# Optimization experiments

Hardware: AMD Instinct MI355X
Metric: run time of the kernel (lower is better)

## Reference

```python
import jax, jax.numpy as jnp
import numpy as np


def setup_inputs() -> dict:
    key = jax.random.key(0)
    k1, k2, k3, k4, k5 = jax.random.split(key, 5)
    B, n_vis, n_hid, n_target = 16384, 2048, 512, 2
    return {
        "input_data": jax.random.normal(k1, (B, n_vis), dtype=jnp.float32),
        "W": jax.random.normal(k2, (n_hid, n_vis), dtype=jnp.float32),
        "U": jax.random.normal(k3, (n_hid, n_target), dtype=jnp.float32),
        "h_bias": jax.random.normal(k4, (1, n_hid), dtype=jnp.float32),
        "y_bias": jax.random.normal(k5, (1, n_target), dtype=jnp.float32),
    }


def reference(input_data, W, U, h_bias, y_bias):
    # precomputed_factor: [B, n_hid]
    pf = input_data @ W.T + h_bias
    # logits[b, c] = y_bias[c] + sum_j softplus(pf[b, j] + U[j, c])
    # broadcast to [B, n_hid, n_target], reduce over hidden dim
    sp = jax.nn.softplus(pf[:, :, None] + U[None, :, :])  # [B, n_hid, n_target]
    logits = y_bias + sp.sum(axis=1)  # [B, n_target]
    # the double class loop computes 1 / sum_d exp(logits_d - logits_c) == softmax
    return jax.nn.softmax(logits, axis=1)
```

## Files before the change

kernel.cpp:

```cpp
#include <hip/hip_runtime.h>
#include <hip/hip_bf16.h>
#include <hip/hip_fp16.h>
#include <stdint.h>

typedef __attribute__((ext_vector_type(8))) _Float16 f16x8;
typedef __attribute__((ext_vector_type(4))) float f32x4;
typedef __attribute__((ext_vector_type(4))) int i32x4;

#define GLD_LDS16(g, l) __builtin_amdgcn_global_load_lds( \
    (const __attribute__((address_space(1))) uint32_t*)(g), \
    (__attribute__((address_space(3))) uint32_t*)(l), 16, 0, 0)

__global__ __launch_bounds__(256) void k_cvt_w(const float* __restrict__ W,
                                               _Float16* __restrict__ Wh) {
  int i = (blockIdx.x * 256 + threadIdx.x) * 8;
  float4 a = *(const float4*)(W + i);
  float4 b = *(const float4*)(W + i + 4);
  union { _Float16 h[8]; i32x4 v; } u;
  u.h[0] = (_Float16)a.x; u.h[1] = (_Float16)a.y;
  u.h[2] = (_Float16)a.z; u.h[3] = (_Float16)a.w;
  u.h[4] = (_Float16)b.x; u.h[5] = (_Float16)b.y;
  u.h[6] = (_Float16)b.z; u.h[7] = (_Float16)b.w;
  *(i32x4*)(Wh + i) = u.v;
}

__device__ inline float softplus_f(float x) {
  float e = __expf(-fabsf(x));
  return fmaxf(x, 0.f) + __logf(1.f + e);
}

__global__ __launch_bounds__(512, 2) void k_main(
    const float* __restrict__ X,
    const _Float16* __restrict__ Wh,
    const float* __restrict__ U,
    const float* __restrict__ hb,
    float* __restrict__ Dp) {
  __shared__ __align__(16) _Float16 As[2][128 * 64];
  __shared__ __align__(16) _Float16 Bs[3][256 * 64];
  __shared__ float sD[128];

  const int t = threadIdx.x;
  const int lane = t & 63;
  const int wid = t >> 6;
  const int wm = wid >> 2;
  const int wn = wid & 3;
  const int bx = blockIdx.x;
  const int rt = (bx >> 4) * 8 + (bx & 7);
  const int nhalf = (bx >> 3) & 1;
  const int bm0 = rt * 128;
  const int bn0 = nhalf * 256;
  const int lrow = lane & 15, lq = lane >> 4;

  if (t < 128) sD[t] = 0.f;
  __syncthreads();

  f32x4 acc[4][4];
#pragma unroll
  for (int m = 0; m < 4; ++m)
#pragma unroll
    for (int n = 0; n < 4; ++n) acc[m][n] = (f32x4){0.f, 0.f, 0.f, 0.f};

  const int arow = t >> 2, ach = t & 3;
  const float* xsrc = X + (size_t)(bm0 + arow) * 2048 + ach * 16;
  const int c0 = ach * 2;
  const int aw0 = arow * 128 + (((c0) ^ (arow & 7)) << 4);
  const int aw1 = arow * 128 + (((c0 + 1) ^ (arow & 7)) << 4);

  const int l8 = lane >> 3, s8 = lane & 7;
  const _Float16* bsrc =
      Wh + (size_t)(bn0 + wid * 32 + l8) * 2048 + (s8 ^ l8) * 8;
  char* const bd0 = (char*)&Bs[0][0] + wid * 4096;
  char* const bd1 = (char*)&Bs[1][0] + wid * 4096;
  char* const bd2 = (char*)&Bs[2][0] + wid * 4096;

  f32x4 arA[4], arB[4];

#define CVT_WRITE_A(ARC, Q) do {                                           \
    f16x8 hv0, hv1;                                                        \
    _Pragma("unroll") for (int j = 0; j < 4; ++j) {                        \
      hv0[j] = (_Float16)ARC[0][j]; hv0[j + 4] = (_Float16)ARC[1][j];      \
      hv1[j] = (_Float16)ARC[2][j]; hv1[j + 4] = (_Float16)ARC[3][j];      \
    }                                                                      \
    *(f16x8*)((char*)&As[Q][0] + aw0) = hv0;                               \
    *(f16x8*)((char*)&As[Q][0] + aw1) = hv1;                               \
  } while (0)

#define STEP(KT, P, Q, ARL, ARC, BR, BWD) do {                             \
    const int kb_ = ((KT) + 2 > 31) ? 31 : (KT) + 2;                       \
    _Pragma("unroll") for (int i = 0; i < 4; ++i)                          \
      GLD_LDS16(bsrc + (size_t)i * 16384 + (size_t)kb_ * 64,               \
                (BWD) + i * 1024);                                         \
    _Pragma("unroll") for (int c = 0; c < 4; ++c)                          \
      ARL[c] = *(const f32x4*)(xsrc + (size_t)kb_ * 64 + c * 4);           \
    CVT_WRITE_A(ARC, Q);                                                   \
    f16x8 fa[4][2], fb[4][2];                                              \
    _Pragma("unroll") for (int mf = 0; mf < 4; ++mf) {                     \
      int row = wm * 64 + mf * 16 + lrow;                                  \
      _Pragma("unroll") for (int ks = 0; ks < 2; ++ks) {                   \
        int off = row * 128 + (((ks * 4 + lq) ^ (row & 7)) << 4);          \
        fa[mf][ks] = *(const f16x8*)((const char*)&As[P][0] + off);        \
      }                                                                    \
    }                                                                      \
    _Pragma("unroll") for (int nf = 0; nf < 4; ++nf) {                     \
      int row = wn * 64 + nf * 16 + lrow;                                  \
      _Pragma("unroll") for (int ks = 0; ks < 2; ++ks) {                   \
        int off = row * 128 + (((ks * 4 + lq) ^ (row & 7)) << 4);          \
        fb[nf][ks] = *(const f16x8*)((const char*)&Bs[BR][0] + off);       \
      }                                                                    \
    }                                                                      \
    _Pragma("unroll") for (int ks = 0; ks < 2; ++ks)                       \
      _Pragma("unroll") for (int mf = 0; mf < 4; ++mf)                     \
        _Pragma("unroll") for (int nf = 0; nf < 4; ++nf)                   \
          acc[mf][nf] = __builtin_amdgcn_mfma_f32_16x16x32_f16(            \
              fa[mf][ks], fb[nf][ks], acc[mf][nf], 0, 0, 0);               \
    asm volatile("s_waitcnt vmcnt(8) lgkmcnt(0)" ::: "memory");            \
    __builtin_amdgcn_s_barrier();                                          \
  } while (0)

#pragma unroll
  for (int i = 0; i < 4; ++i)
    GLD_LDS16(bsrc + (size_t)i * 16384, bd0 + i * 1024);
#pragma unroll
  for (int i = 0; i < 4; ++i)
    GLD_LDS16(bsrc + (size_t)i * 16384 + 64, bd1 + i * 1024);
#pragma unroll
  for (int c = 0; c < 4; ++c) arA[c] = *(const f32x4*)(xsrc + c * 4);
#pragma unroll
  for (int c = 0; c < 4; ++c) arB[c] = *(const f32x4*)(xsrc + 64 + c * 4);
  CVT_WRITE_A(arA, 0);
  asm volatile("s_waitcnt vmcnt(4) lgkmcnt(0)" ::: "memory");
  __builtin_amdgcn_s_barrier();

  for (int kt = 0; kt < 30; kt += 6) {
    STEP(kt + 0, 0, 1, arA, arB, 0, bd2);
    STEP(kt + 1, 1, 0, arB, arA, 1, bd0);
    STEP(kt + 2, 0, 1, arA, arB, 2, bd1);
    STEP(kt + 3, 1, 0, arB, arA, 0, bd2);
    STEP(kt + 4, 0, 1, arA, arB, 1, bd0);
    STEP(kt + 5, 1, 0, arB, arA, 2, bd1);
  }
  STEP(30, 0, 1, arA, arB, 0, bd2);
  STEP(31, 1, 0, arB, arA, 1, bd0);
#undef STEP
#undef CVT_WRITE_A

  float dpart[16];
#pragma unroll
  for (int i = 0; i < 16; ++i) dpart[i] = 0.f;
#pragma unroll
  for (int nf = 0; nf < 4; ++nf) {
    int h = bn0 + wn * 64 + nf * 16 + lrow;
    float hbv = hb[h];
    float u0 = U[2 * h], u1 = U[2 * h + 1];
#pragma unroll
    for (int mf = 0; mf < 4; ++mf)
#pragma unroll
      for (int r = 0; r < 4; ++r) {
        float pf = acc[mf][nf][r] + hbv;
        dpart[mf * 4 + r] += softplus_f(pf + u0) - softplus_f(pf + u1);
      }
  }
#pragma unroll
  for (int i = 0; i < 16; ++i) {
    float v = dpart[i];
    v += __shfl_xor(v, 1);
    v += __shfl_xor(v, 2);
    v += __shfl_xor(v, 4);
    v += __shfl_xor(v, 8);
    dpart[i] = v;
  }
  if (lrow == 0) {
#pragma unroll
    for (int mf = 0; mf < 4; ++mf)
#pragma unroll
      for (int r = 0; r < 4; ++r)
        atomicAdd(&sD[wm * 64 + mf * 16 + lq * 4 + r], dpart[mf * 4 + r]);
  }
  __syncthreads();
  if (t < 128) Dp[nhalf * 16384 + bm0 + t] = sD[t];
}

__global__ __launch_bounds__(256) void k_final(const float* __restrict__ Dp,
                                               const float* __restrict__ yb,
                                               float* __restrict__ out) {
  int i = blockIdx.x * 256 + threadIdx.x;
  float D = Dp[i] + Dp[16384 + i] + yb[0] - yb[1];
  float e = __expf(-D);
  float o0 = 1.f / (1.f + e);
  float o1 = e * o0;
  *(float2*)(out + (size_t)i * 2) = make_float2(o0, o1);
}

extern "C" void kernel_launch(void* const* d_in, const int* in_sizes, int n_in,
                              void* d_out, int out_size, void* d_ws,
                              size_t ws_size, hipStream_t stream) {
  const float* X = (const float*)d_in[0];
  const float* W = (const float*)d_in[1];
  const float* U = (const float*)d_in[2];
  const float* hb = (const float*)d_in[3];
  const float* yb = (const float*)d_in[4];
  float* out = (float*)d_out;
  _Float16* Wh = (_Float16*)d_ws;
  float* Dp = (float*)((char*)d_ws + 2 * 1024 * 1024);

  hipLaunchKernelGGL(k_cvt_w, dim3(512), dim3(256), 0, stream, W, Wh);
  hipLaunchKernelGGL(k_main, dim3(256), dim3(512), 0, stream, X, Wh, U, hb, Dp);
  hipLaunchKernelGGL(k_final, dim3(64), dim3(256), 0, stream, Dp, yb, out);
}
```

Before: 67.86 us.

## Shrink main GEMM tile to 128x128 with K-step 32, doubling block count

Changes the main fused kernel from 512-thread blocks computing 128x256 tiles with K=64 steps to 256-thread blocks computing 128x128 tiles with K=32 steps. The grid doubles to 512 blocks, and the LDS swizzle is rebuilt for 64-byte rows. The final kernel now sums four partial softplus-difference buffers. The aim is more blocks for the 256 CUs and better occupancy. The cost is that X is read and converted twice as many times, and each K-step has more barrier overhead.

```diff
diff --git a/kernel.cpp b/kernel.cpp
--- a/kernel.cpp
+++ b/kernel.cpp
@@ -29,26 +29,26 @@
   return fmaxf(x, 0.f) + __logf(1.f + e);
 }
 
-__global__ __launch_bounds__(512, 2) void k_main(
+__global__ __launch_bounds__(256, 3) void k_main(
     const float* __restrict__ X,
     const _Float16* __restrict__ Wh,
     const float* __restrict__ U,
     const float* __restrict__ hb,
     float* __restrict__ Dp) {
-  __shared__ __align__(16) _Float16 As[2][128 * 64];
-  __shared__ __align__(16) _Float16 Bs[3][256 * 64];
+  __shared__ __align__(16) _Float16 As[2][128 * 32];
+  __shared__ __align__(16) _Float16 Bs[3][128 * 32];
   __shared__ float sD[128];
 
   const int t = threadIdx.x;
   const int lane = t & 63;
   const int wid = t >> 6;
-  const int wm = wid >> 2;
-  const int wn = wid & 3;
+  const int wm = wid >> 1;
+  const int wn = wid & 1;
   const int bx = blockIdx.x;
-  const int rt = (bx >> 4) * 8 + (bx & 7);
-  const int nhalf = (bx >> 3) & 1;
+  const int rt = (bx >> 5) * 8 + (bx & 7);
+  const int nq = (bx >> 3) & 3;
   const int bm0 = rt * 128;
-  const int bn0 = nhalf * 256;
+  const int bn0 = nq * 128;
   const int lrow = lane & 15, lq = lane >> 4;
 
   if (t < 128) sD[t] = 0.f;
@@ -60,18 +60,19 @@
 #pragma unroll
     for (int n = 0; n < 4; ++n) acc[m][n] = (f32x4){0.f, 0.f, 0.f, 0.f};
 
-  const int arow = t >> 2, ach = t & 3;
-  const float* xsrc = X + (size_t)(bm0 + arow) * 2048 + ach * 16;
-  const int c0 = ach * 2;
-  const int aw0 = arow * 128 + (((c0) ^ (arow & 7)) << 4);
-  const int aw1 = arow * 128 + (((c0 + 1) ^ (arow & 7)) << 4);
-
-  const int l8 = lane >> 3, s8 = lane & 7;
+  const int arow = t >> 1;
+  const float* xsrc = X + (size_t)(bm0 + arow) * 2048 + (t & 1) * 16;
+  const int c0 = (t & 1) * 2;
+  const int aw0 = arow * 64 + (((c0 + (arow >> 1)) & 3) << 4);
+  const int aw1 = arow * 64 + (((c0 + 1 + (arow >> 1)) & 3) << 4);
+
+  const int brow = lane >> 2;
+  const int bchunk = ((lane & 3) - ((lane >> 3) & 3)) & 3;
   const _Float16* bsrc =
-      Wh + (size_t)(bn0 + wid * 32 + l8) * 2048 + (s8 ^ l8) * 8;
-  char* const bd0 = (char*)&Bs[0][0] + wid * 4096;
-  char* const bd1 = (char*)&Bs[1][0] + wid * 4096;
-  char* const bd2 = (char*)&Bs[2][0] + wid * 4096;
+      Wh + (size_t)(bn0 + wid * 32 + brow) * 2048 + bchunk * 8;
+  char* const bd0 = (char*)&Bs[0][0] + wid * 2048;
+  char* const bd1 = (char*)&Bs[1][0] + wid * 2048;
+  char* const bd2 = (char*)&Bs[2][0] + wid * 2048;
 
   f32x4 arA[4], arB[4];
 
@@ -86,52 +87,44 @@
   } while (0)
 
 #define STEP(KT, P, Q, ARL, ARC, BR, BWD) do {                             \
-    const int kb_ = ((KT) + 2 > 31) ? 31 : (KT) + 2;                       \
-    _Pragma("unroll") for (int i = 0; i < 4; ++i)                          \
-      GLD_LDS16(bsrc + (size_t)i * 16384 + (size_t)kb_ * 64,               \
-                (BWD) + i * 1024);                                         \
+    const int kb_ = ((KT) + 2 > 63) ? 63 : (KT) + 2;                       \
+    GLD_LDS16(bsrc + (size_t)kb_ * 32, (BWD));                             \
+    GLD_LDS16(bsrc + (size_t)16 * 2048 + (size_t)kb_ * 32, (BWD) + 1024);  \
     _Pragma("unroll") for (int c = 0; c < 4; ++c)                          \
-      ARL[c] = *(const f32x4*)(xsrc + (size_t)kb_ * 64 + c * 4);           \
+      ARL[c] = *(const f32x4*)(xsrc + (size_t)kb_ * 32 + c * 4);           \
     CVT_WRITE_A(ARC, Q);                                                   \
-    f16x8 fa[4][2], fb[4][2];                                              \
+    f16x8 fa[4], fb[4];                                                    \
     _Pragma("unroll") for (int mf = 0; mf < 4; ++mf) {                     \
       int row = wm * 64 + mf * 16 + lrow;                                  \
-      _Pragma("unroll") for (int ks = 0; ks < 2; ++ks) {                   \
-        int off = row * 128 + (((ks * 4 + lq) ^ (row & 7)) << 4);          \
-        fa[mf][ks] = *(const f16x8*)((const char*)&As[P][0] + off);        \
-      }                                                                    \
+      fa[mf] = *(const f16x8*)((const char*)&As[P][0] + row * 64 +         \
+                               (((lq + (row >> 1)) & 3) << 4));            \
     }                                                                      \
     _Pragma("unroll") for (int nf = 0; nf < 4; ++nf) {                     \
       int row = wn * 64 + nf * 16 + lrow;                                  \
-      _Pragma("unroll") for (int ks = 0; ks < 2; ++ks) {                   \
-        int off = row * 128 + (((ks * 4 + lq) ^ (row & 7)) << 4);          \
-        fb[nf][ks] = *(const f16x8*)((const char*)&Bs[BR][0] + off);       \
-      }                                                                    \
+      fb[nf] = *(const f16x8*)((const char*)&Bs[BR][0] + row * 64 +        \
+                               (((lq + (row >> 1)) & 3) << 4));            \
     }                                                                      \
-    _Pragma("unroll") for (int ks = 0; ks < 2; ++ks)                       \
-      _Pragma("unroll") for (int mf = 0; mf < 4; ++mf)                     \
-        _Pragma("unroll") for (int nf = 0; nf < 4; ++nf)                   \
-          acc[mf][nf] = __builtin_amdgcn_mfma_f32_16x16x32_f16(            \
-              fa[mf][ks], fb[nf][ks], acc[mf][nf], 0, 0, 0);               \
-    asm volatile("s_waitcnt vmcnt(8) lgkmcnt(0)" ::: "memory");            \
+    _Pragma("unroll") for (int mf = 0; mf < 4; ++mf)                       \
+      _Pragma("unroll") for (int nf = 0; nf < 4; ++nf)                     \
+        acc[mf][nf] = __builtin_amdgcn_mfma_f32_16x16x32_f16(              \
+            fa[mf], fb[nf], acc[mf][nf], 0, 0, 0);                         \
+    asm volatile("s_waitcnt vmcnt(6) lgkmcnt(0)" ::: "memory");            \
     __builtin_amdgcn_s_barrier();                                          \
   } while (0)
 
-#pragma unroll
-  for (int i = 0; i < 4; ++i)
-    GLD_LDS16(bsrc + (size_t)i * 16384, bd0 + i * 1024);
-#pragma unroll
-  for (int i = 0; i < 4; ++i)
-    GLD_LDS16(bsrc + (size_t)i * 16384 + 64, bd1 + i * 1024);
+  GLD_LDS16(bsrc, bd0);
+  GLD_LDS16(bsrc + (size_t)16 * 2048, bd0 + 1024);
+  GLD_LDS16(bsrc + 32, bd1);
+  GLD_LDS16(bsrc + (size_t)16 * 2048 + 32, bd1 + 1024);
 #pragma unroll
   for (int c = 0; c < 4; ++c) arA[c] = *(const f32x4*)(xsrc + c * 4);
 #pragma unroll
-  for (int c = 0; c < 4; ++c) arB[c] = *(const f32x4*)(xsrc + 64 + c * 4);
+  for (int c = 0; c < 4; ++c) arB[c] = *(const f32x4*)(xsrc + 32 + c * 4);
   CVT_WRITE_A(arA, 0);
   asm volatile("s_waitcnt vmcnt(4) lgkmcnt(0)" ::: "memory");
   __builtin_amdgcn_s_barrier();
 
-  for (int kt = 0; kt < 30; kt += 6) {
+  for (int kt = 0; kt < 60; kt += 6) {
     STEP(kt + 0, 0, 1, arA, arB, 0, bd2);
     STEP(kt + 1, 1, 0, arB, arA, 1, bd0);
     STEP(kt + 2, 0, 1, arA, arB, 2, bd1);
@@ -139,8 +132,10 @@
     STEP(kt + 4, 0, 1, arA, arB, 1, bd0);
     STEP(kt + 5, 1, 0, arB, arA, 2, bd1);
   }
-  STEP(30, 0, 1, arA, arB, 0, bd2);
-  STEP(31, 1, 0, arB, arA, 1, bd0);
+  STEP(60, 0, 1, arA, arB, 0, bd2);
+  STEP(61, 1, 0, arB, arA, 1, bd0);
+  STEP(62, 0, 1, arA, arB, 2, bd1);
+  STEP(63, 1, 0, arB, arA, 0, bd2);
 #undef STEP
 #undef CVT_WRITE_A
 
@@ -177,14 +172,15 @@
         atomicAdd(&sD[wm * 64 + mf * 16 + lq * 4 + r], dpart[mf * 4 + r]);
   }
   __syncthreads();
-  if (t < 128) Dp[nhalf * 16384 + bm0 + t] = sD[t];
+  if (t < 128) Dp[nq * 16384 + bm0 + t] = sD[t];
 }
 
 __global__ __launch_bounds__(256) void k_final(const float* __restrict__ Dp,
                                                const float* __restrict__ yb,
                                                float* __restrict__ out) {
   int i = blockIdx.x * 256 + threadIdx.x;
-  float D = Dp[i] + Dp[16384 + i] + yb[0] - yb[1];
+  float D = Dp[i] + Dp[16384 + i] + Dp[2 * 16384 + i] + Dp[3 * 16384 + i] +
+            yb[0] - yb[1];
   float e = __expf(-D);
   float o0 = 1.f / (1.f + e);
   float o1 = e * o0;
@@ -204,6 +200,7 @@
   float* Dp = (float*)((char*)d_ws + 2 * 1024 * 1024);
 
   hipLaunchKernelGGL(k_cvt_w, dim3(512), dim3(256), 0, stream, W, Wh);
-  hipLaunchKernelGGL(k_main, dim3(256), dim3(512), 0, stream, X, Wh, U, hb, Dp);
+  hipLaunchKernelGGL(k_main, dim3(512), dim3(256), 0, stream, X, Wh, U, hb,
+                     Dp);
   hipLaunchKernelGGL(k_final, dim3(64), dim3(256), 0, stream, Dp, yb, out);
 }
```

After: 81.72 us. 1.2x slower.

## Split each K step into two phases with setprio-ping-ponged MFMA clusters

Applied to the files above, without the earlier changes.

Each K-tile step is split into two half-steps (ks=0 and ks=1). Each half-step loads its own fragments, issues global loads or the A convert/write, then runs 16 MFMAs wrapped in s_setprio(1). Extra s_barriers and sched_barriers are added so the two waves per SIMD alternate between memory and MFMA phases, aiming to overlap LDS and global traffic with matrix math. The cost is four barriers per step instead of one, which adds synchronization overhead, and tighter fragment register use.

```diff
diff --git a/kernel.cpp b/kernel.cpp
--- a/kernel.cpp
+++ b/kernel.cpp
@@ -85,36 +85,54 @@
     *(f16x8*)((char*)&As[Q][0] + aw1) = hv1;                               \
   } while (0)
 
+#define FRAGS(P, BR, KS, FA, FB) do {                                      \
+    _Pragma("unroll") for (int mf = 0; mf < 4; ++mf) {                     \
+      int row = wm * 64 + mf * 16 + lrow;                                  \
+      int off = row * 128 + ((((KS)*4 + lq) ^ (row & 7)) << 4);            \
+      FA[mf] = *(const f16x8*)((const char*)&As[P][0] + off);              \
+    }                                                                      \
+    _Pragma("unroll") for (int nf = 0; nf < 4; ++nf) {                     \
+      int row = wn * 64 + nf * 16 + lrow;                                  \
+      int off = row * 128 + ((((KS)*4 + lq) ^ (row & 7)) << 4);            \
+      FB[nf] = *(const f16x8*)((const char*)&Bs[BR][0] + off);             \
+    }                                                                      \
+  } while (0)
+
+#define MFMA16(FA, FB) do {                                                \
+    __builtin_amdgcn_s_setprio(1);                                         \
+    _Pragma("unroll") for (int mf = 0; mf < 4; ++mf)                       \
+      _Pragma("unroll") for (int nf = 0; nf < 4; ++nf)                     \
+        acc[mf][nf] = __builtin_amdgcn_mfma_f32_16x16x32_f16(              \
+            FA[mf], FB[nf], acc[mf][nf], 0, 0, 0);                         \
+    __builtin_amdgcn_s_setprio(0);                                         \
+  } while (0)
+
 #define STEP(KT, P, Q, ARL, ARC, BR, BWD) do {                             \
     const int kb_ = ((KT) + 2 > 31) ? 31 : (KT) + 2;                       \
-    _Pragma("unroll") for (int i = 0; i < 4; ++i)                          \
-      GLD_LDS16(bsrc + (size_t)i * 16384 + (size_t)kb_ * 64,               \
-                (BWD) + i * 1024);                                         \
-    _Pragma("unroll") for (int c = 0; c < 4; ++c)                          \
-      ARL[c] = *(const f32x4*)(xsrc + (size_t)kb_ * 64 + c * 4);           \
-    CVT_WRITE_A(ARC, Q);                                                   \
-    f16x8 fa[4][2], fb[4][2];                                              \
-    _Pragma("unroll") for (int mf = 0; mf < 4; ++mf) {                     \
-      int row = wm * 64 + mf * 16 + lrow;                                  \
-      _Pragma("unroll") for (int ks = 0; ks < 2; ++ks) {                   \
-        int off = row * 128 + (((ks * 4 + lq) ^ (row & 7)) << 4);          \
-        fa[mf][ks] = *(const f16x8*)((const char*)&As[P][0] + off);        \
-      }                                                                    \
-    }                                                                      \
-    _Pragma("unroll") for (int nf = 0; nf < 4; ++nf) {                     \
-      int row = wn * 64 + nf * 16 + lrow;                                  \
-      _Pragma("unroll") for (int ks = 0; ks < 2; ++ks) {                   \
-        int off = row * 128 + (((ks * 4 + lq) ^ (row & 7)) << 4);          \
-        fb[nf][ks] = *(const f16x8*)((const char*)&Bs[BR][0] + off);       \
-      }                                                                    \
-    }                                                                      \
-    _Pragma("unroll") for (int ks = 0; ks < 2; ++ks)                       \
-      _Pragma("unroll") for (int mf = 0; mf < 4; ++mf)                     \
-        _Pragma("unroll") for (int nf = 0; nf < 4; ++nf)                   \
-          acc[mf][nf] = __builtin_amdgcn_mfma_f32_16x16x32_f16(            \
-              fa[mf][ks], fb[nf][ks], acc[mf][nf], 0, 0, 0);               \
-    asm volatile("s_waitcnt vmcnt(8) lgkmcnt(0)" ::: "memory");            \
-    __builtin_amdgcn_s_barrier();                                          \
+    {                  \
+      f16x8 fa[4], fb[4];                                                  \
+      FRAGS(P, BR, 0, fa, fb);                                             \
+      _Pragma("unroll") for (int i = 0; i < 4; ++i)                        \
+        GLD_LDS16(bsrc + (size_t)i * 16384 + (size_t)kb_ * 64,             \
+                  (BWD) + i * 1024);                                       \
+      __builtin_amdgcn_s_barrier();                                        \
+      asm volatile("s_waitcnt lgkmcnt(0)" ::: "memory");                   \
+      __builtin_amdgcn_sched_barrier(0);                                   \
+      MFMA16(fa, fb);                                                      \
+      __builtin_amdgcn_s_barrier();                                        \
+    }                                                                      \
+    {       \
+      f16x8 fa[4], fb[4];                                                  \
+      FRAGS(P, BR, 1, fa, fb);                                             \
+      _Pragma("unroll") for (int c = 0; c < 4; ++c)                        \
+        ARL[c] = *(const f32x4*)(xsrc + (size_t)kb_ * 64 + c * 4);         \
+      CVT_WRITE_A(ARC, Q);                                                 \
+      asm volatile("s_waitcnt vmcnt(8) lgkmcnt(0)" ::: "memory");          \
+      __builtin_amdgcn_sched_barrier(0);                                   \
+      __builtin_amdgcn_s_barrier();                                        \
+      MFMA16(fa, fb);                                                      \
+      __builtin_amdgcn_s_barrier();                                        \
+    }                                                                      \
   } while (0)
 
 #pragma unroll
@@ -142,6 +160,8 @@
   STEP(30, 0, 1, arA, arB, 0, bd2);
   STEP(31, 1, 0, arB, arA, 1, bd0);
 #undef STEP
+#undef MFMA16
+#undef FRAGS
 #undef CVT_WRITE_A
 
   float dpart[16];
```

New measurement: 64.29 us. -5.3%, faster.
